# Kernel tuning notes

Measured on AMD Instinct MI355X. Metric: run time of the kernel, lower is better.

Reference implementation:

```python
import jax, jax.numpy as jnp
import numpy as np

N_NODES = 100000
N_EDGES = 1600000
IN_DIM = 256
OUT_DIM = 128
NEG_SLOPE = 0.2
LAMBDA = 0.5  # fixed (non-learnable), clamped to [0,1] in original
EPS = 1e-8


def setup_inputs() -> dict:
    key = jax.random.key(0)
    ks = jax.random.split(key, 8)
    x = jax.random.normal(ks[0], (N_NODES, IN_DIM), dtype=jnp.float32)
    edge_index = jax.random.randint(ks[1], (2, N_EDGES), 0, N_NODES, dtype=jnp.int64)
    beta = jax.random.uniform(ks[2], (N_EDGES,), dtype=jnp.float32)
    # Learned parameters (xavier-scale random instead of the zero init so the
    # attention path is exercised numerically).
    s_gat = (6.0 / (IN_DIM + OUT_DIM)) ** 0.5
    W_gat = jax.random.uniform(ks[3], (OUT_DIM, IN_DIM), jnp.float32, -s_gat, s_gat)
    att_src = jax.random.normal(ks[4], (OUT_DIM,), dtype=jnp.float32) * 0.1
    att_dst = jax.random.normal(ks[5], (OUT_DIM,), dtype=jnp.float32) * 0.1
    bias = jnp.zeros((OUT_DIM,), dtype=jnp.float32)
    W_fixed = jax.random.uniform(ks[6], (OUT_DIM, IN_DIM), jnp.float32, -s_gat, s_gat)
    return {
        "x": x, "edge_index": edge_index, "beta": beta,
        "W_gat": W_gat, "att_src": att_src, "att_dst": att_dst,
        "bias": bias, "W_fixed": W_fixed,
    }


def reference(x, edge_index, beta, W_gat, att_src, att_dst, bias, W_fixed):
    N = x.shape[0]
    src, dst = edge_index[0], edge_index[1]

    # ---- STAGATE attention branch (hL) ----
    h = x @ W_gat.T                       # (N, D)
    h_src = h[src]                        # (E, D) gather
    h_dst = h[dst]                        # (E, D) gather
    e = h_src @ att_src + h_dst @ att_dst # (E,)
    e = jnp.where(e >= 0, e, NEG_SLOPE * e)   # LeakyReLU
    alpha = jax.nn.sigmoid(e)
    denom = jax.ops.segment_sum(alpha, dst, num_segments=N) + EPS  # (N,)
    alpha = alpha / denom[dst]
    hL = jax.ops.segment_sum(h_src * alpha[:, None], dst, num_segments=N)
    hL = hL + bias

    # ---- fixed-beta branch (hF) ----
    xW = x @ W_fixed.T                    # (N, D)
    hF = jax.ops.segment_sum(xW[src] * beta[:, None], dst, num_segments=N)

    # ---- fuse + activation ----
    lam = jnp.clip(jnp.float32(LAMBDA), 0.0, 1.0)
    out = lam * hL + (1.0 - lam) * hF
    return jax.nn.elu(out)
```

## Files before the change

### kernel.cpp

```cpp
#include <hip/hip_runtime.h>
#include <math.h>

#define N_NODES 100000
#define N_EDGES 1600000
#define IN_DIM 256
#define OUT_DIM 128
#define NEG_SLOPE 0.2f
#define LAMBDA 0.5f
#define EPS 1e-8f

#define FIX_SCALE 67108864.0f
#define FIX_INV   (1.0f / 67108864.0f)
#define CNT_SHIFT 46

#define OFF_HXB   ((size_t)0)
#define OFF_WC    ((size_t)12800000)
#define OFF_ASRC  ((size_t)12832768)
#define OFF_ADST  ((size_t)12932768)
#define OFF_PACK  ((size_t)13032768)
#define OFF_COUNT ((size_t)13232768)
#define OFF_OFFS  ((size_t)13332768)
#define OFF_BSUM  ((size_t)13432768)
#define OFF_TMP   ((size_t)13433792)
#define OFF_REC   ((size_t)19833792)
#define WS_FLOATS ((size_t)26233792)

#define SCAN_BLOCKS ((N_NODES + 255) / 256)

typedef __attribute__((ext_vector_type(8))) short bf16x8;
typedef __attribute__((ext_vector_type(4))) float f32x4;

__device__ __forceinline__ unsigned short f2b(float f) {
    unsigned u = __float_as_uint(f);
    u += 0x7FFFu + ((u >> 16) & 1u);
    return (unsigned short)(u >> 16);
}
__device__ __forceinline__ float b2f_lo(unsigned u) { return __uint_as_float(u << 16); }
__device__ __forceinline__ float b2f_hi(unsigned u) { return __uint_as_float(u & 0xFFFF0000u); }

__global__ __launch_bounds__(256) void convert_w2(
    const float* __restrict__ Wg, const float* __restrict__ Wf,
    ushort* __restrict__ Wc2)
{
    int g  = blockIdx.x * 256 + threadIdx.x;
    int n  = g & 255;
    int kb = g >> 8;
    const float* src = (n < 128) ? (Wg + (size_t)n * 256 + kb * 8)
                                 : (Wf + (size_t)(n - 128) * 256 + kb * 8);
    float4 a = *(const float4*)(src);
    float4 b = *(const float4*)(src + 4);
    ushort p[8];
    p[0] = f2b(a.x); p[1] = f2b(a.y); p[2] = f2b(a.z); p[3] = f2b(a.w);
    p[4] = f2b(b.x); p[5] = f2b(b.y); p[6] = f2b(b.z); p[7] = f2b(b.w);
    *(bf16x8*)(Wc2 + (size_t)g * 8) = *(bf16x8*)p;
}

__global__ __launch_bounds__(256) void gemm_mfma(
    const float* __restrict__ x, const ushort* __restrict__ Wc2,
    const float* __restrict__ att_s, const float* __restrict__ att_d,
    ushort* __restrict__ hxb,
    float* __restrict__ a_src, float* __restrict__ a_dst)
{
    __shared__ ushort As[64 * 264];
    __shared__ ushort Bs[4 * 256 * 8];
    const int tid  = threadIdx.x;
    const int wv   = tid >> 6;
    const int lane = tid & 63;
    const int quad = lane >> 4;
    const int l16  = lane & 15;
    const int nb   = blockIdx.x * 64;

    f32x4 acc[4][4];
#pragma unroll
    for (int mt = 0; mt < 4; ++mt)
#pragma unroll
        for (int nt = 0; nt < 4; ++nt) acc[mt][nt] = (f32x4){0.f, 0.f, 0.f, 0.f};

#pragma unroll
    for (int it = 0; it < 16; ++it) {
        int f   = tid + it * 256;
        int row = f >> 6;
        int c4  = (f & 63) << 2;
        int gn  = nb + row; if (gn >= N_NODES) gn = N_NODES - 1;
        float4 v = *(const float4*)(x + (size_t)gn * IN_DIM + c4);
        ushort4 p;
        p.x = f2b(v.x); p.y = f2b(v.y); p.z = f2b(v.z); p.w = f2b(v.w);
        *(ushort4*)(&As[row * 264 + c4]) = p;
    }

    for (int kc = 0; kc < 256; kc += 32) {
        __syncthreads();
#pragma unroll
        for (int it = 0; it < 4; ++it) {
            int off = (it * 256 + tid) * 8;
            *(bf16x8*)(&Bs[off]) = *(const bf16x8*)(Wc2 + (size_t)kc * 256 + off);
        }
        __syncthreads();

        bf16x8 afr[4], bfr[4];
#pragma unroll
        for (int mt = 0; mt < 4; ++mt)
            afr[mt] = *(const bf16x8*)(&As[(mt * 16 + l16) * 264 + kc + quad * 8]);
#pragma unroll
        for (int nt = 0; nt < 4; ++nt) {
            int n = (wv & 1) * 64 + ((wv >> 1) << 7) + nt * 16 + l16;
            bfr[nt] = *(const bf16x8*)(&Bs[((size_t)quad * 256 + n) * 8]);
        }
#pragma unroll
        for (int mt = 0; mt < 4; ++mt)
#pragma unroll
            for (int nt = 0; nt < 4; ++nt)
                acc[mt][nt] = __builtin_amdgcn_mfma_f32_16x16x32_bf16(
                    afr[mt], bfr[nt], acc[mt][nt], 0, 0, 0);
    }

    __syncthreads();
    {
        const int colbase = (wv >> 1) * 128 + (wv & 1) * 64;
#pragma unroll
        for (int mt = 0; mt < 4; ++mt)
#pragma unroll
            for (int nt = 0; nt < 4; ++nt) {
                int col = colbase + nt * 16 + l16;
#pragma unroll
                for (int r = 0; r < 4; ++r)
                    As[(mt * 16 + quad * 4 + r) * 264 + col] = f2b(acc[mt][nt][r]);
            }
    }
    __syncthreads();

    {
        const int row = tid >> 2;
        const int q   = tid & 3;
        const int gn  = nb + row;
        bf16x8 v[8];
#pragma unroll
        for (int j = 0; j < 8; ++j)
            v[j] = *(const bf16x8*)(&As[row * 264 + q * 64 + j * 8]);
        if (gn < N_NODES) {
            ushort* dst = hxb + (size_t)gn * 256 + q * 64;
#pragma unroll
            for (int j = 0; j < 8; ++j)
                *(bf16x8*)(dst + j * 8) = v[j];
        }
        if (q < 2) {
            const float4* as4 = (const float4*)att_s;
            const float4* ad4 = (const float4*)att_d;
            float ss = 0.f, dd = 0.f;
#pragma unroll
            for (int j = 0; j < 8; ++j) {
#pragma unroll
                for (int hv = 0; hv < 2; ++hv) {
                    float4 sa = as4[q * 16 + j * 2 + hv];
                    float4 da = ad4[q * 16 + j * 2 + hv];
                    unsigned u0 = ((const unsigned*)&v[j])[hv * 2];
                    unsigned u1 = ((const unsigned*)&v[j])[hv * 2 + 1];
                    float f0 = b2f_lo(u0), f1 = b2f_hi(u0), f2 = b2f_lo(u1), f3 = b2f_hi(u1);
                    ss += f0 * sa.x + f1 * sa.y + f2 * sa.z + f3 * sa.w;
                    dd += f0 * da.x + f1 * da.y + f2 * da.z + f3 * da.w;
                }
            }
            ss += __shfl_xor(ss, 1);
            dd += __shfl_xor(dd, 1);
            if (q == 0 && gn < N_NODES) { a_src[gn] = ss; a_dst[gn] = dd; }
        }
    }
}

__global__ __launch_bounds__(256) void edge_prep(
    const int* __restrict__ ei, const float* __restrict__ a_src,
    const float* __restrict__ a_dst, unsigned long long* __restrict__ pack,
    int4* __restrict__ tmp)
{
    const int bb = blockIdx.x * 1024 + threadIdx.x;
#pragma unroll
    for (int k = 0; k < 4; ++k) {
        int e = bb + k * 256;
        if (e >= N_EDGES) break;
        int s = ei[e];
        int d = ei[N_EDGES + e];
        s = s < 0 ? 0 : (s >= N_NODES ? N_NODES - 1 : s);
        d = d < 0 ? 0 : (d >= N_NODES ? N_NODES - 1 : d);
        float ev = a_src[s] + a_dst[d];
        ev = ev >= 0.f ? ev : NEG_SLOPE * ev;
        float al = 1.f / (1.f + __expf(-ev));
        unsigned fix = (unsigned)(al * FIX_SCALE + 0.5f);
        unsigned long long old = atomicAdd(pack + d,
            ((unsigned long long)1 << CNT_SHIFT) | (unsigned long long)fix);
        int pos = (int)(old >> CNT_SHIFT);
        tmp[e] = make_int4(s, d, pos, __float_as_int(al));
    }
}

__global__ __launch_bounds__(256) void scan1(
    const unsigned long long* __restrict__ pack, int* __restrict__ count,
    int* __restrict__ offs, int* __restrict__ bsum)
{
    __shared__ int s[256];
    int i = blockIdx.x * 256 + threadIdx.x;
    int v = (i < N_NODES) ? (int)(pack[i] >> CNT_SHIFT) : 0;
    if (i < N_NODES) count[i] = v;
    s[threadIdx.x] = v;
    __syncthreads();
    for (int off = 1; off < 256; off <<= 1) {
        int t = (threadIdx.x >= off) ? s[threadIdx.x - off] : 0;
        __syncthreads();
        s[threadIdx.x] += t;
        __syncthreads();
    }
    if (i < N_NODES) offs[i] = s[threadIdx.x] - v;
    if (threadIdx.x == 255) bsum[blockIdx.x] = s[255];
}

__global__ __launch_bounds__(512) void scan2(int* __restrict__ bsum)
{
    __shared__ int s[512];
    int v = (threadIdx.x < SCAN_BLOCKS) ? bsum[threadIdx.x] : 0;
    s[threadIdx.x] = v;
    __syncthreads();
    for (int off = 1; off < 512; off <<= 1) {
        int t = (threadIdx.x >= off) ? s[threadIdx.x - off] : 0;
        __syncthreads();
        s[threadIdx.x] += t;
        __syncthreads();
    }
    if (threadIdx.x < SCAN_BLOCKS) bsum[threadIdx.x] = s[threadIdx.x] - v;
}

__global__ __launch_bounds__(256) void scatter_rec(
    const int4* __restrict__ tmp, const unsigned long long* __restrict__ pack,
    const int* __restrict__ offs, const int* __restrict__ bsum,
    const float* __restrict__ beta, float4* __restrict__ rec)
{
    int e = blockIdx.x * 256 + threadIdx.x;
    int4 t = tmp[e];
    float al = __int_as_float(t.w);
    unsigned long long p = pack[t.y];
    float denom = (float)(p & (((unsigned long long)1 << CNT_SHIFT) - 1)) * FIX_INV;
    float c1 = LAMBDA * al / (denom + EPS);
    float c2 = (1.f - LAMBDA) * beta[e];
    int slot = offs[t.y] + bsum[t.y >> 8] + t.z;
    rec[slot] = make_float4(__int_as_float(t.x), c1, c2, 0.f);
}

#define ACC8(u, c)                                              \
    av[0] += (c) * b2f_lo((u).x); av[1] += (c) * b2f_hi((u).x); \
    av[2] += (c) * b2f_lo((u).y); av[3] += (c) * b2f_hi((u).y); \
    av[4] += (c) * b2f_lo((u).z); av[5] += (c) * b2f_hi((u).z); \
    av[6] += (c) * b2f_lo((u).w); av[7] += (c) * b2f_hi((u).w);

__global__ __launch_bounds__(256) void segment_reduce(
    const ushort* __restrict__ hxb,
    const float4* __restrict__ rec, const int* __restrict__ offs,
    const int* __restrict__ bsum, const int* __restrict__ count,
    const float* __restrict__ bias, float* __restrict__ out)
{
    int wave = (blockIdx.x * 256 + threadIdx.x) >> 6;
    int lane = threadIdx.x & 63;
    if (wave >= N_NODES) return;
    const int start = offs[wave] + bsum[wave >> 8];
    const int cnt   = count[wave];
    const int sub  = lane >> 5;
    const int half = (lane >> 4) & 1;
    const int li   = lane & 15;
    const ushort* __restrict__ base = hxb + half * 128 + li * 8;

    float av[8] = {0.f, 0.f, 0.f, 0.f, 0.f, 0.f, 0.f, 0.f};
    int k = 0;
    for (; k + 8 <= cnt; k += 8) {
        float4 rA = rec[start + k + sub];
        float4 rB = rec[start + k + 2 + sub];
        float4 rC = rec[start + k + 4 + sub];
        float4 rD = rec[start + k + 6 + sub];
        uint4 uA = *(const uint4*)(base + (size_t)__float_as_int(rA.x) * 256);
        uint4 uB = *(const uint4*)(base + (size_t)__float_as_int(rB.x) * 256);
        uint4 uC = *(const uint4*)(base + (size_t)__float_as_int(rC.x) * 256);
        uint4 uD = *(const uint4*)(base + (size_t)__float_as_int(rD.x) * 256);
        float cA = half ? rA.z : rA.y;
        float cB = half ? rB.z : rB.y;
        float cC = half ? rC.z : rC.y;
        float cD = half ? rD.z : rD.y;
        ACC8(uA, cA); ACC8(uB, cB); ACC8(uC, cC); ACC8(uD, cD);
    }
    for (; k + 4 <= cnt; k += 4) {
        float4 rA = rec[start + k + sub];
        float4 rB = rec[start + k + 2 + sub];
        uint4 uA = *(const uint4*)(base + (size_t)__float_as_int(rA.x) * 256);
        uint4 uB = *(const uint4*)(base + (size_t)__float_as_int(rB.x) * 256);
        float cA = half ? rA.z : rA.y;
        float cB = half ? rB.z : rB.y;
        ACC8(uA, cA); ACC8(uB, cB);
    }
    for (; k < cnt; k += 2) {
        int kk  = k + sub;
        int idx = start + (kk < cnt ? kk : cnt - 1);
        float4 r = rec[idx];
        float c = half ? r.z : r.y;
        c = (kk < cnt) ? c : 0.f;
        uint4 u = *(const uint4*)(base + (size_t)__float_as_int(r.x) * 256);
        ACC8(u, c);
    }

#pragma unroll
    for (int j = 0; j < 8; ++j) av[j] += __shfl_xor(av[j], 32);
#pragma unroll
    for (int j = 0; j < 8; ++j) av[j] += __shfl_xor(av[j], 16);

    if (lane < 16) {
        const float4* b4 = (const float4*)(bias + li * 8);
        float4 b0 = b4[0], b1 = b4[1];
        float o[8];
        o[0] = av[0] + LAMBDA * b0.x; o[1] = av[1] + LAMBDA * b0.y;
        o[2] = av[2] + LAMBDA * b0.z; o[3] = av[3] + LAMBDA * b0.w;
        o[4] = av[4] + LAMBDA * b1.x; o[5] = av[5] + LAMBDA * b1.y;
        o[6] = av[6] + LAMBDA * b1.z; o[7] = av[7] + LAMBDA * b1.w;
#pragma unroll
        for (int j = 0; j < 8; ++j) o[j] = o[j] > 0.f ? o[j] : expm1f(o[j]);
        float* op = out + (size_t)wave * OUT_DIM + li * 8;
        *(float4*)(op)     = make_float4(o[0], o[1], o[2], o[3]);
        *(float4*)(op + 4) = make_float4(o[4], o[5], o[6], o[7]);
    }
}

extern "C" void kernel_launch(void* const* d_in, const int* in_sizes, int n_in,
                              void* d_out, int out_size, void* d_ws, size_t ws_size,
                              hipStream_t stream)
{
    const float* x     = (const float*)d_in[0];
    const int*   ei    = (const int*)d_in[1];
    const float* beta  = (const float*)d_in[2];
    const float* Wg    = (const float*)d_in[3];
    const float* att_s = (const float*)d_in[4];
    const float* att_d = (const float*)d_in[5];
    const float* bias  = (const float*)d_in[6];
    const float* Wf    = (const float*)d_in[7];
    float* out = (float*)d_out;
    float* ws  = (float*)d_ws;

    if (ws_size < WS_FLOATS * sizeof(float)) return;

    ushort* hxb  = (ushort*)(ws + OFF_HXB);
    ushort* Wc2  = (ushort*)(ws + OFF_WC);
    float*  asrc = ws + OFF_ASRC;
    float*  adst = ws + OFF_ADST;
    unsigned long long* pack = (unsigned long long*)(ws + OFF_PACK);
    int*    count = (int*)(ws + OFF_COUNT);
    int*    offs  = (int*)(ws + OFF_OFFS);
    int*    bsum  = (int*)(ws + OFF_BSUM);
    int4*   tmp   = (int4*)(ws + OFF_TMP);
    float4* rec   = (float4*)(ws + OFF_REC);

    hipMemsetAsync(pack, 0, (size_t)N_NODES * sizeof(unsigned long long), stream);

    convert_w2<<<32, 256, 0, stream>>>(Wg, Wf, Wc2);
    gemm_mfma<<<(N_NODES + 63) / 64, 256, 0, stream>>>(x, Wc2, att_s, att_d, hxb, asrc, adst);
    edge_prep<<<(N_EDGES + 1023) / 1024, 256, 0, stream>>>(ei, asrc, adst, pack, tmp);
    scan1<<<SCAN_BLOCKS, 256, 0, stream>>>(pack, count, offs, bsum);
    scan2<<<1, 512, 0, stream>>>(bsum);
    scatter_rec<<<N_EDGES / 256, 256, 0, stream>>>(tmp, pack, offs, bsum, beta, rec);
    segment_reduce<<<(N_NODES * 64 + 255) / 256, 256, 0, stream>>>(hxb, rec, offs, bsum, count, bias, out);
}
```

Before: 477.3 us.

## Software-pipeline segment_reduce edge loop with double-buffered record and gather loads

Restructures the per-node edge loop in segment_reduce into a software pipeline. Record loads for the next batch and row gathers for the current batch are issued before accumulating the previous batch, using two register sets (A/B). The separate tail loops are replaced by index clamping and zeroed coefficients. The aim is to hide gather latency. In exchange it uses more registers, which may lower occupancy, and it does redundant loads at the tail.

```diff
diff --git a/kernel.cpp b/kernel.cpp
--- a/kernel.cpp
+++ b/kernel.cpp
@@ -249,6 +249,30 @@
     av[4] += (c) * b2f_lo((u).z); av[5] += (c) * b2f_hi((u).z); \
     av[6] += (c) * b2f_lo((u).w); av[7] += (c) * b2f_hi((u).w);
 
+#define LOADN(b) {                                              \
+    int i0 = (b) + sub,     i1 = (b) + 2 + sub;                 \
+    int i2 = (b) + 4 + sub, i3 = (b) + 6 + sub;                 \
+    i0 = i0 > last ? last : i0;  i1 = i1 > last ? last : i1;    \
+    i2 = i2 > last ? last : i2;  i3 = i3 > last ? last : i3;    \
+    n0 = rp[i0]; n1 = rp[i1]; n2 = rp[i2]; n3 = rp[i3]; }
+
+#define COMMIT(S, b) {                                                        \
+    s##S##0 = __float_as_int(n0.x); s##S##1 = __float_as_int(n1.x);           \
+    s##S##2 = __float_as_int(n2.x); s##S##3 = __float_as_int(n3.x);           \
+    c##S##0 = ((b) + sub     < cnt) ? (half ? n0.z : n0.y) : 0.f;             \
+    c##S##1 = ((b) + 2 + sub < cnt) ? (half ? n1.z : n1.y) : 0.f;             \
+    c##S##2 = ((b) + 4 + sub < cnt) ? (half ? n2.z : n2.y) : 0.f;             \
+    c##S##3 = ((b) + 6 + sub < cnt) ? (half ? n3.z : n3.y) : 0.f; }
+
+#define GATHER(S) {                                                           \
+    g##S##0 = *(const uint4*)(base + (size_t)s##S##0 * 256);                  \
+    g##S##1 = *(const uint4*)(base + (size_t)s##S##1 * 256);                  \
+    g##S##2 = *(const uint4*)(base + (size_t)s##S##2 * 256);                  \
+    g##S##3 = *(const uint4*)(base + (size_t)s##S##3 * 256); }
+
+#define ACCSET(S) { ACC8(g##S##0, c##S##0); ACC8(g##S##1, c##S##1);           \
+                    ACC8(g##S##2, c##S##2); ACC8(g##S##3, c##S##3); }
+
 __global__ __launch_bounds__(256) void segment_reduce(
     const ushort* __restrict__ hxb,
     const float4* __restrict__ rec, const int* __restrict__ offs,
@@ -266,39 +290,41 @@
     const ushort* __restrict__ base = hxb + half * 128 + li * 8;
 
     float av[8] = {0.f, 0.f, 0.f, 0.f, 0.f, 0.f, 0.f, 0.f};
-    int k = 0;
-    for (; k + 8 <= cnt; k += 8) {
-        float4 rA = rec[start + k + sub];
-        float4 rB = rec[start + k + 2 + sub];
-        float4 rC = rec[start + k + 4 + sub];
-        float4 rD = rec[start + k + 6 + sub];
-        uint4 uA = *(const uint4*)(base + (size_t)__float_as_int(rA.x) * 256);
-        uint4 uB = *(const uint4*)(base + (size_t)__float_as_int(rB.x) * 256);
-        uint4 uC = *(const uint4*)(base + (size_t)__float_as_int(rC.x) * 256);
-        uint4 uD = *(const uint4*)(base + (size_t)__float_as_int(rD.x) * 256);
-        float cA = half ? rA.z : rA.y;
-        float cB = half ? rB.z : rB.y;
-        float cC = half ? rC.z : rC.y;
-        float cD = half ? rD.z : rD.y;
-        ACC8(uA, cA); ACC8(uB, cB); ACC8(uC, cC); ACC8(uD, cD);
-    }
-    for (; k + 4 <= cnt; k += 4) {
-        float4 rA = rec[start + k + sub];
-        float4 rB = rec[start + k + 2 + sub];
-        uint4 uA = *(const uint4*)(base + (size_t)__float_as_int(rA.x) * 256);
-        uint4 uB = *(const uint4*)(base + (size_t)__float_as_int(rB.x) * 256);
-        float cA = half ? rA.z : rA.y;
-        float cB = half ? rB.z : rB.y;
-        ACC8(uA, cA); ACC8(uB, cB);
-    }
-    for (; k < cnt; k += 2) {
-        int kk  = k + sub;
-        int idx = start + (kk < cnt ? kk : cnt - 1);
-        float4 r = rec[idx];
-        float c = half ? r.z : r.y;
-        c = (kk < cnt) ? c : 0.f;
-        uint4 u = *(const uint4*)(base + (size_t)__float_as_int(r.x) * 256);
-        ACC8(u, c);
+
+    if (cnt > 0) {
+        const float4* __restrict__ rp = rec + start;
+        const int last = cnt - 1;
+        const int T = (cnt + 7) >> 3;
+
+        float4 n0, n1, n2, n3;
+        int   sA0, sA1, sA2, sA3,  sB0, sB1, sB2, sB3;
+        float cA0, cA1, cA2, cA3,  cB0, cB1, cB2, cB3;
+        uint4 gA0, gA1, gA2, gA3,  gB0, gB1, gB2, gB3;
+
+        LOADN(0); COMMIT(A, 0);
+        GATHER(A);
+        if (T == 1) {
+            ACCSET(A);
+        } else {
+            LOADN(8); COMMIT(B, 8);
+            int j = 1, b = 8;
+            while (true) {
+                LOADN(b + 8);
+                GATHER(B);
+                ACCSET(A);
+                COMMIT(A, b + 8);
+                ++j;
+                if (j >= T) { ACCSET(B); break; }
+                b += 8;
+                LOADN(b + 8);
+                GATHER(A);
+                ACCSET(B);
+                COMMIT(B, b + 8);
+                ++j;
+                if (j >= T) { ACCSET(A); break; }
+                b += 8;
+            }
+        }
     }
 
 #pragma unroll
```

Result: slower. 497.4 us (+4.2%).
